# Performance work log

Measured on AMD Instinct MI355X. Metric: run time of the kernel, lower is better.

The kernel has to match this reference:

```python
import jax, jax.numpy as jnp
import numpy as np

B, L, H, SH, C = 32, 512, 1024, 50, 3   # batch, leaves, hidden, hidden_syn_size, num_classes
N = 2 * L - 1                            # total tree nodes (complete binary / heap order)
VOCAB, SYN = 30000, 128
LVLS = int(np.log2(L))                   # number of internal levels (root = level 0)


def _linear(k, fin, fout):
    lim = 1.0 / np.sqrt(fin)
    kw, kb = jax.random.split(k)
    W = jax.random.uniform(kw, (fin, fout), minval=-lim, maxval=lim, dtype=jnp.float32)
    b = jax.random.uniform(kb, (fout,), minval=-lim, maxval=lim, dtype=jnp.float32)
    return W, b


def setup_inputs() -> dict:
    key = jax.random.key(0)
    ks = jax.random.split(key, 12)
    x = jax.random.randint(ks[0], (B, N), 0, SYN)                 # node ids (word at leaves, syntax elsewhere)
    word_index = jnp.broadcast_to(jnp.arange(L - 1, 2 * L - 1), (B, L))  # leaf node indices (heap order)
    cue = jax.random.randint(ks[1], (B, N), 0, C)
    pos = jax.random.randint(ks[2], (B, L), 0, SYN)               # POS tag per leaf
    # parent->child adjacency of the heap tree, adj[:,1] is what forward reads
    A = np.zeros((N, N), dtype=bool)
    par = np.arange(L - 1)
    A[par, 2 * par + 1] = True
    A[par, 2 * par + 2] = True
    adj = jnp.broadcast_to(jnp.asarray(A)[None, None], (B, 2, N, N))
    pre_embs = jnp.zeros((1,), jnp.float32)                       # unused (use_pretrained_embs=False)
    word_emb_W = jax.random.normal(ks[3], (VOCAB, H), jnp.float32) * 0.02
    syn_emb_W = jax.random.normal(ks[4], (SYN, SH), jnp.float32) * 0.02
    leaf_W, leaf_b = _linear(ks[5], H + SH + C, H)
    comp_W, comp_b = _linear(ks[6], 2 * H + SH, H)
    grev_W, grev_b = _linear(ks[7], H + SH, H)
    dec_W, dec_b = _linear(ks[8], 2 * H + 2 * SH, 2 * H)
    clf_W, clf_b = _linear(ks[9], 2 * H, C)
    return dict(x=x, word_index=word_index, cue=cue, adj=adj, pos=pos, pre_embs=pre_embs,
                word_emb_W=word_emb_W, syn_emb_W=syn_emb_W,
                leaf_W=leaf_W, leaf_b=leaf_b, comp_W=comp_W, comp_b=comp_b,
                grev_W=grev_W, grev_b=grev_b, dec_W=dec_W, dec_b=dec_b,
                clf_W=clf_W, clf_b=clf_b)


def reference(x, word_index, cue, adj, pos, pre_embs,
              word_emb_W, syn_emb_W, leaf_W, leaf_b, comp_W, comp_b,
              grev_W, grev_b, dec_W, dec_b, clf_W, clf_b):
    # Eval-mode forward (self.training == False, so no dropout masks are applied).
    # Tree structure is the complete binary heap encoded in adj: children of i are 2i+1, 2i+2.
    b_ix = jnp.arange(B)[:, None]
    s = jnp.take_along_axis(x, word_index, axis=1)                # (B,L) leaf word ids
    c = jnp.take_along_axis(cue, word_index, axis=1)              # (B,L) leaf cue ids
    word_e = word_emb_W[s]                                        # (B,L,H)
    cue_e = jax.nn.one_hot(c, C, dtype=word_e.dtype)              # (B,L,C)
    pos_e = syn_emb_W[pos]                                        # (B,L,SH)
    x_emb = jnp.concatenate([word_e, cue_e, pos_e], -1) @ leaf_W + leaf_b  # (B,L,H), no activation

    up = jnp.zeros((B, N, H), x_emb.dtype).at[b_ix, word_index].set(x_emb)
    # upward pass: batched level-order compose (bottom internal level -> root)
    for lvl in range(LVLS - 1, -1, -1):
        nodes = jnp.arange(2 ** lvl - 1, 2 ** (lvl + 1) - 1)
        l, r = 2 * nodes + 1, 2 * nodes + 2
        cons = syn_emb_W[x[:, nodes]]                             # (B,W,SH)
        ctx = jnp.concatenate([cons, up[:, l], up[:, r]], -1)     # (B,W,SH+2H)
        up = up.at[:, nodes].set(jnp.tanh(ctx @ comp_W + comp_b))

    root_ctx = jnp.concatenate([up[:, 0], syn_emb_W[x[:, 0]]], -1)
    gd = jnp.tanh(root_ctx @ grev_W + grev_b)                     # (B,H)
    down = jnp.zeros((B, N, H), gd.dtype).at[:, 0].set(gd)
    # downward pass: batched level-order decompose (root -> leaves)
    for lvl in range(LVLS):
        nodes = jnp.arange(2 ** lvl - 1, 2 ** (lvl + 1) - 1)
        l, r = 2 * nodes + 1, 2 * nodes + 2
        if lvl == LVLS - 1:   # children are leaves -> their syntax is the POS embedding
            cons_l = pos_e[:, l - (L - 1)]
            cons_r = pos_e[:, r - (L - 1)]
        else:
            cons_l = syn_emb_W[x[:, l]]
            cons_r = syn_emb_W[x[:, r]]
        pctx = jnp.concatenate([down[:, nodes], up[:, nodes]], -1)  # (parent_emb, upward[parent])
        dctx = jnp.concatenate([cons_l, cons_r, pctx], -1)
        ch = jnp.tanh(dctx @ dec_W + dec_b)                        # (B,W,2H)
        down = down.at[:, l].set(ch[..., :H]).at[:, r].set(ch[..., H:])

    tree = jnp.concatenate([down, up], -1)                         # (B,N,2H)
    return jnp.tanh(tree @ clf_W + clf_b)                          # (B,N,C)
```

## Files before the change

kernel.cpp:

```cpp
#include <hip/hip_runtime.h>

typedef unsigned short u16;
typedef unsigned int   u32;

typedef __bf16 bf16x8 __attribute__((ext_vector_type(8)));
typedef float  f32x4  __attribute__((ext_vector_type(4)));

#define NB 1023
#define HH 1024

__device__ __forceinline__ float b2f(u16 x) { return __uint_as_float(((u32)x) << 16); }
__device__ __forceinline__ u16 f2b(float f) {
    u32 u = __float_as_uint(f);
    u += 0x7fffu + ((u >> 16) & 1u);
    return (u16)(u >> 16);
}
__device__ __forceinline__ float fast_tanh(float x) {
    float cx = fminf(fmaxf(x, -12.f), 12.f);
    float e = __expf(2.f * cx);
    return __fdividef(e - 1.f, e + 1.f);
}
__device__ __forceinline__ void async_copy16(const void* gptr, void* lptr) {
    __builtin_amdgcn_global_load_lds((__attribute__((address_space(1))) void*)gptr,
                                     (__attribute__((address_space(3))) void*)lptr,
                                     16, 0, 0);
}
__device__ __forceinline__ u16 loadAsBf16(const void* p, size_t idx, int isf32) {
    if (isf32) return f2b(((const float*)p)[idx]);
    return ((const u16*)p)[idx];
}

__device__ __forceinline__ int detect_local(const u32* __restrict__ w) {
    __shared__ int cnt;
    const int tid = threadIdx.x;
    if (tid == 0) cnt = 0;
    __syncthreads();
    u32 v = w[tid & 255];
    u32 lo = v & 0xFFFFu;
    u32 e = (lo >> 7) & 0xFFu;
    if ((lo != 0u) && (e < 60u || e > 140u)) atomicAdd(&cnt, 1);
    __syncthreads();
    return cnt >= 64;
}

__device__ void conv_range(const void* __restrict__ src, u16* __restrict__ dst,
                           int n, int tbase, int isf32) {
    const int i = ((int)blockIdx.x - tbase) * 256 + threadIdx.x;
    if (i < n) dst[i] = loadAsBf16(src, i, isf32);
}

__device__ void transpose_tile(const void* __restrict__ W, u16* __restrict__ Wt,
                               int Nw, int Kpad, int bx, int by, int isf32,
                               int ps0, int ps1, int ps2, int ps3,
                               int os0, int os1, int os2, int os3,
                               int ln0, int ln1, int ln2, int ln3)
{
    __shared__ u16 tile[32][33];
    const int tid = threadIdx.x;
    const int tx = tid & 31, ty = tid >> 5;
    #pragma unroll
    for (int i = 0; i < 4; ++i) {
        const int kp = by*32 + ty + i*8;
        const int n = bx*32 + tx;
        int ko = -1;
        if      (kp >= ps0 && kp < ps0 + ln0) ko = os0 + (kp - ps0);
        else if (kp >= ps1 && kp < ps1 + ln1) ko = os1 + (kp - ps1);
        else if (kp >= ps2 && kp < ps2 + ln2) ko = os2 + (kp - ps2);
        else if (kp >= ps3 && kp < ps3 + ln3) ko = os3 + (kp - ps3);
        u16 v = 0;
        if (ko >= 0) v = loadAsBf16(W, (size_t)ko * Nw + n, isf32);
        tile[ty + i*8][tx] = v;
    }
    __syncthreads();
    #pragma unroll
    for (int i = 0; i < 4; ++i) {
        const int n = bx*32 + ty + i*8;
        const int kp = by*32 + tx;
        Wt[(size_t)n * Kpad + kp] = tile[tx][ty + i*8];
    }
}

__global__ __launch_bounds__(256)
void preprocess(const u32* __restrict__ wembU,
                const int* __restrict__ x, const int* __restrict__ cue,
                const int* __restrict__ pos,
                const void* __restrict__ semb,  const void* __restrict__ leafb,
                const void* __restrict__ compb, const void* __restrict__ grevb,
                const void* __restrict__ decb,  const void* __restrict__ clfb,
                const void* __restrict__ clfW,
                const void* __restrict__ leafW, const void* __restrict__ compW,
                const void* __restrict__ grevW, const void* __restrict__ decW,
                u16* __restrict__ sembP,  u16* __restrict__ leafbC,
                u16* __restrict__ compbC, u16* __restrict__ grevbC,
                u16* __restrict__ decbC,  u16* __restrict__ clfbC,
                u16* __restrict__ clfWC,
                u16* __restrict__ leafWt, u16* __restrict__ compWt,
                u16* __restrict__ grevWt, u16* __restrict__ decWt,
                u16* __restrict__ ctx)
{
    const int isf32 = detect_local(wembU);
    const int bid = blockIdx.x;
    if (bid < 32) {
        const int i = bid * 256 + threadIdx.x;
        const int s = i >> 6, c = i & 63;
        sembP[i] = (c < 50) ? loadAsBf16(semb, s * 50 + c, isf32) : (u16)0;
    } else if (bid < 36)  conv_range(leafb, leafbC, 1024, 32, isf32);
    else if (bid < 40)  conv_range(compb, compbC, 1024, 36, isf32);
    else if (bid < 44)  conv_range(grevb, grevbC, 1024, 40, isf32);
    else if (bid < 52)  conv_range(decb,  decbC,  2048, 44, isf32);
    else if (bid < 53)  conv_range(clfb,  clfbC,  3,    52, isf32);
    else if (bid < 77)  conv_range(clfW,  clfWC,  6144, 53, isf32);
    else if (bid < 1165) {
        const int t = bid - 77;
        transpose_tile(leafW, leafWt, 1024, 1088, t & 31, t >> 5, isf32,
                       0,-1,-1,-1,  0,0,0,0,  1077,0,0,0);
    } else if (bid < 3277) {
        const int t = bid - 1165;
        transpose_tile(compW, compWt, 1024, 2112, t & 31, t >> 5, isf32,
                       0,64,1088,-1,  0,50,1074,0,  50,1024,1024,0);
    } else if (bid < 4365) {
        const int t = bid - 3277;
        transpose_tile(grevW, grevWt, 1024, 1088, t & 31, t >> 5, isf32,
                       0,1024,-1,-1,  0,1024,0,0,  1024,50,0,0);
    } else if (bid < 8717) {
        const int t = bid - 4365;
        transpose_tile(decW, decWt, 2048, 2176, t & 63, t >> 6, isf32,
                       0,64,128,1152,  0,50,100,1124,  50,50,1024,1024);
    } else {
        const int m = bid - 8717;
        const int b = m >> 9, i = m & 511;
        const int node = 511 + i;
        const int s  = x[b*NB + node];
        const int cv = cue[b*NB + node];
        const int p  = pos[b*512 + i];
        u16* row = ctx + (size_t)m * 1088;
        u32* row32 = (u32*)row;
        const int tid = threadIdx.x;
        if (isf32) {
            const float2* wrf = ((const float2*)wembU) + (size_t)s * 512;
            for (int c = tid; c < 512; c += 256) {
                float2 t = wrf[c];
                row32[c] = (u32)f2b(t.x) | ((u32)f2b(t.y) << 16);
            }
        } else {
            const u32* wr = ((const u32*)wembU) + (size_t)s * 512;
            for (int c = tid; c < 512; c += 256) row32[c] = wr[c];
        }
        if (tid < 64) {
            const int c = tid;
            u16 v;
            if (c < 3)       v = (c == cv) ? (u16)0x3F80 : (u16)0;
            else if (c < 53) v = loadAsBf16(semb, p * 50 + (c - 3), isf32);
            else             v = 0;
            row[1024 + c] = v;
        }
    }
}

template<int AKIND>
__device__ __forceinline__ void setup_arows(
    int mrow, int M, int nodeBase, int lognn, int mask, int leafLvl, int scol, int Kpad,
    const u16* __restrict__ actx, const int* __restrict__ x, const int* __restrict__ pos,
    const u16* __restrict__ sembP, const u16* __restrict__ upB, const u16* __restrict__ downB,
    const u16*& q0, const u16*& q1, const u16*& q2, const u16*& q3)
{
    const int mr = (mrow < M) ? mrow : 0;
    if (AKIND == 0) {
        q0 = actx + (size_t)mr * Kpad + scol;
    } else if (AKIND == 1) {
        const int b_ = mr >> lognn, ii = mr & mask;
        const int node = nodeBase + ii;
        const int s = x[b_*NB + node];
        q0 = sembP + s*64 + scol;
        q1 = upB + (((size_t)(b_*NB + 2*node + 1)) << 10) + scol;
        q2 = upB + (((size_t)(b_*NB + 2*node + 2)) << 10) + scol;
    } else if (AKIND == 2) {
        q0 = upB + (((size_t)(mr*NB)) << 10) + scol;
        q1 = sembP + x[mr*NB]*64 + scol;
    } else {
        const int b_ = mr >> lognn, ii = mr & mask;
        const int node = nodeBase + ii;
        const int l = 2*node + 1, r = l + 1;
        int sli, sri;
        if (leafLvl) { sli = pos[b_*512 + (l-511)]; sri = pos[b_*512 + (r-511)]; }
        else         { sli = x[b_*NB + l]; sri = x[b_*NB + r]; }
        q0 = sembP + sli*64 + scol;
        q1 = sembP + sri*64 + scol;
        q2 = downB + (((size_t)(b_*NB + node)) << 10) + scol;
        q3 = upB   + (((size_t)(b_*NB + node)) << 10) + scol;
    }
}

template<int AKIND, int MODE>
__global__ __launch_bounds__(256)
void gemm_fused(const u16* __restrict__ Bt, const u16* __restrict__ bias,
                u16* __restrict__ dst, int M, int Kpad, int nodeBase, int lognn,
                int leafLvl,
                const u16* __restrict__ actx,
                const int* __restrict__ x, const int* __restrict__ pos,
                const u16* __restrict__ sembP,
                const u16* __restrict__ upB, const u16* __restrict__ downB)
{
    __shared__ __align__(16) u16 As[2*4096];
    __shared__ __align__(16) u16 Bs[2*4096];
    const int tid  = threadIdx.x;
    const int wave = tid >> 6;
    const int lane = tid & 63;
    const int bm = blockIdx.y << 7;
    const int bn = blockIdx.x << 7;
    const int wm = (wave & 1) << 6;
    const int wn = (wave >> 1) << 6;
    const int quad = lane >> 4;
    const int l16  = lane & 15;
    const int srow = lane >> 2;
    const int scol = (lane & 3) << 3;
    const int mask = (1 << lognn) - 1;

    const u16 *p0[2], *p1[2], *p2[2], *p3[2];
    #pragma unroll
    for (int h = 0; h < 2; ++h)
        setup_arows<AKIND>(bm + wave*16 + srow + h*64, M, nodeBase, lognn, mask, leafLvl,
                           scol, Kpad, actx, x, pos, sembP, upB, downB,
                           p0[h], p1[h], p2[h], p3[h]);

    const u16* gB0 = Bt + (size_t)(bn + wave*16 + srow) * Kpad + scol;
    const u16* gB1 = gB0 + (size_t)64 * Kpad;
    u16* lA0 = &As[wave * 512];
    u16* lA1 = &As[(wave + 4) * 512];
    u16* lB0 = &Bs[wave * 512];
    u16* lB1 = &Bs[(wave + 4) * 512];

    const u16* pa[4]; const u16* pb[4];
    #pragma unroll
    for (int i = 0; i < 4; ++i) pa[i] = &As[(wm + i*16 + l16) * 32 + quad*8];
    #pragma unroll
    for (int j = 0; j < 4; ++j) pb[j] = &Bs[(wn + j*16 + l16) * 32 + quad*8];

    f32x4 zero4 = {0.f, 0.f, 0.f, 0.f};
    f32x4 acc[4][4];
    #pragma unroll
    for (int i = 0; i < 4; ++i)
        #pragma unroll
        for (int j = 0; j < 4; ++j) acc[i][j] = zero4;

    auto kstep64 = [&](const u16* sA0, const u16* sA1, int k0) {
        async_copy16(sA0,           lA0);
        async_copy16(sA1,           lA1);
        async_copy16(gB0 + k0,      lB0);
        async_copy16(gB1 + k0,      lB1);
        async_copy16(sA0 + 32,      lA0 + 4096);
        async_copy16(sA1 + 32,      lA1 + 4096);
        async_copy16(gB0 + k0 + 32, lB0 + 4096);
        async_copy16(gB1 + k0 + 32, lB1 + 4096);
        __syncthreads();
        #pragma unroll
        for (int c = 0; c < 2; ++c) {
            bf16x8 a[4], b[4];
            #pragma unroll
            for (int i = 0; i < 4; ++i) a[i] = *(const bf16x8*)(pa[i] + c*4096);
            #pragma unroll
            for (int j = 0; j < 4; ++j) b[j] = *(const bf16x8*)(pb[j] + c*4096);
            #pragma unroll
            for (int i = 0; i < 4; ++i)
                #pragma unroll
                for (int j = 0; j < 4; ++j)
                    acc[i][j] = __builtin_amdgcn_mfma_f32_16x16x32_bf16(a[i], b[j], acc[i][j], 0, 0, 0);
        }
        __syncthreads();
    };

    if (AKIND == 0) {
        for (int k0 = 0; k0 < 1088; k0 += 64) kstep64(p0[0] + k0, p0[1] + k0, k0);
    } else if (AKIND == 1) {
        kstep64(p0[0], p0[1], 0);
        for (int k0 = 64;   k0 < 1088; k0 += 64) kstep64(p1[0] + (k0-64),   p1[1] + (k0-64),   k0);
        for (int k0 = 1088; k0 < 2112; k0 += 64) kstep64(p2[0] + (k0-1088), p2[1] + (k0-1088), k0);
    } else if (AKIND == 2) {
        for (int k0 = 0; k0 < 1024; k0 += 64) kstep64(p0[0] + k0, p0[1] + k0, k0);
        kstep64(p1[0], p1[1], 1024);
    } else {
        kstep64(p0[0], p0[1], 0);
        kstep64(p1[0], p1[1], 64);
        for (int k0 = 128;  k0 < 1152; k0 += 64) kstep64(p2[0] + (k0-128),  p2[1] + (k0-128),  k0);
        for (int k0 = 1152; k0 < 2176; k0 += 64) kstep64(p3[0] + (k0-1152), p3[1] + (k0-1152), k0);
    }

    #pragma unroll
    for (int i = 0; i < 4; ++i) {
        #pragma unroll
        for (int j = 0; j < 4; ++j) {
            const int gn = bn + wn + j*16 + l16;
            const float bv = b2f(bias[gn]);
            #pragma unroll
            for (int r = 0; r < 4; ++r) {
                const int gm = bm + wm + i*16 + quad*4 + r;
                if (gm < M) {
                    float v = acc[i][j][r] + bv;
                    if (MODE != 0) v = fast_tanh(v);
                    const int b_ = gm >> lognn;
                    const int ii = gm & mask;
                    const int node = nodeBase + ii;
                    size_t addr;
                    if (MODE == 2) {
                        const int child = 2*node + 1 + (gn >> 10);
                        addr = (((size_t)(b_*NB + child)) << 10) + (gn & 1023);
                    } else {
                        addr = (((size_t)(b_*NB + node)) << 10) + gn;
                    }
                    dst[addr] = f2b(v);
                }
            }
        }
    }
}

template<int AKIND, int MODE>
__global__ __launch_bounds__(256, 2)
void gemm_wide(const u16* __restrict__ Bt, const u16* __restrict__ bias,
               u16* __restrict__ dst, int M, int Kpad, int nodeBase, int lognn,
               int leafLvl,
               const u16* __restrict__ actx,
               const int* __restrict__ x, const int* __restrict__ pos,
               const u16* __restrict__ sembP,
               const u16* __restrict__ upB, const u16* __restrict__ downB)
{
    __shared__ __align__(16) u16 As[2*4096];
    __shared__ __align__(16) u16 Bs[2*8192];
    const int tid  = threadIdx.x;
    const int wave = tid >> 6;
    const int lane = tid & 63;
    const int bm = blockIdx.y << 7;
    const int bn = blockIdx.x << 8;
    const int wm = (wave & 1) << 6;
    const int wn = (wave >> 1) << 7;
    const int quad = lane >> 4;
    const int l16  = lane & 15;
    const int srow = lane >> 2;
    const int scol = (lane & 3) << 3;
    const int mask = (1 << lognn) - 1;

    const u16 *p0[2], *p1[2], *p2[2], *p3[2];
    #pragma unroll
    for (int h = 0; h < 2; ++h)
        setup_arows<AKIND>(bm + wave*16 + srow + h*64, M, nodeBase, lognn, mask, leafLvl,
                           scol, Kpad, actx, x, pos, sembP, upB, downB,
                           p0[h], p1[h], p2[h], p3[h]);

    const u16* gB[4];
    #pragma unroll
    for (int g = 0; g < 4; ++g)
        gB[g] = Bt + (size_t)(bn + wave*64 + g*16 + srow) * Kpad + scol;
    u16* lA0 = &As[wave * 512];
    u16* lA1 = &As[(wave + 4) * 512];
    u16* lB[4];
    #pragma unroll
    for (int g = 0; g < 4; ++g) lB[g] = &Bs[wave * 2048 + g * 512];

    const u16* pa[4]; const u16* pb[8];
    #pragma unroll
    for (int i = 0; i < 4; ++i) pa[i] = &As[(wm + i*16 + l16) * 32 + quad*8];
    #pragma unroll
    for (int j = 0; j < 8; ++j) pb[j] = &Bs[(wn + j*16 + l16) * 32 + quad*8];

    f32x4 zero4 = {0.f, 0.f, 0.f, 0.f};
    f32x4 acc[4][8];
    #pragma unroll
    for (int i = 0; i < 4; ++i)
        #pragma unroll
        for (int j = 0; j < 8; ++j) acc[i][j] = zero4;

    auto kstep64 = [&](const u16* sA0, const u16* sA1, int k0) {
        async_copy16(sA0,      lA0);
        async_copy16(sA1,      lA1);
        #pragma unroll
        for (int g = 0; g < 4; ++g) async_copy16(gB[g] + k0, lB[g]);
        async_copy16(sA0 + 32, lA0 + 4096);
        async_copy16(sA1 + 32, lA1 + 4096);
        #pragma unroll
        for (int g = 0; g < 4; ++g) async_copy16(gB[g] + k0 + 32, lB[g] + 8192);
        __syncthreads();
        #pragma unroll
        for (int c = 0; c < 2; ++c) {
            bf16x8 a[4], b[8];
            #pragma unroll
            for (int i = 0; i < 4; ++i) a[i] = *(const bf16x8*)(pa[i] + c*4096);
            #pragma unroll
            for (int j = 0; j < 8; ++j) b[j] = *(const bf16x8*)(pb[j] + c*8192);
            #pragma unroll
            for (int i = 0; i < 4; ++i)
                #pragma unroll
                for (int j = 0; j < 8; ++j)
                    acc[i][j] = __builtin_amdgcn_mfma_f32_16x16x32_bf16(a[i], b[j], acc[i][j], 0, 0, 0);
        }
        __syncthreads();
    };

    if (AKIND == 0) {
        for (int k0 = 0; k0 < 1088; k0 += 64) kstep64(p0[0] + k0, p0[1] + k0, k0);
    } else if (AKIND == 1) {
        kstep64(p0[0], p0[1], 0);
        for (int k0 = 64;   k0 < 1088; k0 += 64) kstep64(p1[0] + (k0-64),   p1[1] + (k0-64),   k0);
        for (int k0 = 1088; k0 < 2112; k0 += 64) kstep64(p2[0] + (k0-1088), p2[1] + (k0-1088), k0);
    } else if (AKIND == 2) {
        for (int k0 = 0; k0 < 1024; k0 += 64) kstep64(p0[0] + k0, p0[1] + k0, k0);
        kstep64(p1[0], p1[1], 1024);
    } else {
        kstep64(p0[0], p0[1], 0);
        kstep64(p1[0], p1[1], 64);
        for (int k0 = 128;  k0 < 1152; k0 += 64) kstep64(p2[0] + (k0-128),  p2[1] + (k0-128),  k0);
        for (int k0 = 1152; k0 < 2176; k0 += 64) kstep64(p3[0] + (k0-1152), p3[1] + (k0-1152), k0);
    }

    #pragma unroll
    for (int i = 0; i < 4; ++i) {
        #pragma unroll
        for (int j = 0; j < 8; ++j) {
            const int gn = bn + wn + j*16 + l16;
            const float bv = b2f(bias[gn]);
            #pragma unroll
            for (int r = 0; r < 4; ++r) {
                const int gm = bm + wm + i*16 + quad*4 + r;
                if (gm < M) {
                    float v = acc[i][j][r] + bv;
                    if (MODE != 0) v = fast_tanh(v);
                    const int b_ = gm >> lognn;
                    const int ii = gm & mask;
                    const int node = nodeBase + ii;
                    size_t addr;
                    if (MODE == 2) {
                        const int child = 2*node + 1 + (gn >> 10);
                        addr = (((size_t)(b_*NB + child)) << 10) + (gn & 1023);
                    } else {
                        addr = (((size_t)(b_*NB + node)) << 10) + gn;
                    }
                    dst[addr] = f2b(v);
                }
            }
        }
    }
}

__global__ __launch_bounds__(256)
void classifier_kernel(const u16* __restrict__ down, const u16* __restrict__ up,
                       const u16* __restrict__ clfW, const u16* __restrict__ clfb,
                       void* __restrict__ outp, const u32* __restrict__ wembU)
{
    __shared__ float wls[3][2048];
    const int isf32 = detect_local(wembU);
    const int tid = threadIdx.x;
    for (int idx = tid; idx < 6144; idx += 256) {
        const int c = idx >> 11, k = idx & 2047;
        wls[c][k] = b2f(clfW[k*3 + c]);
    }
    __syncthreads();
    const int wave = tid >> 6, lane = tid & 63;
    const float b0 = b2f(clfb[0]), b1 = b2f(clfb[1]), b2v = b2f(clfb[2]);
    const int base = blockIdx.x * 32;
    for (int rr = 0; rr < 8; ++rr) {
        const int row = base + rr*4 + wave;
        const u32* dn = (const u32*)(down + ((size_t)row << 10));
        const u32* un = (const u32*)(up   + ((size_t)row << 10));
        float a0 = 0.f, a1 = 0.f, a2 = 0.f;
        #pragma unroll
        for (int t = 0; t < 8; ++t) {
            const int j = t*64 + lane;
            const u32 dp = dn[j], uu = un[j];
            const int k = j*2;
            const float d0 = __uint_as_float(dp << 16);
            const float d1 = __uint_as_float(dp & 0xffff0000u);
            const float u0 = __uint_as_float(uu << 16);
            const float u1 = __uint_as_float(uu & 0xffff0000u);
            a0 += d0*wls[0][k] + d1*wls[0][k+1] + u0*wls[0][1024+k] + u1*wls[0][1025+k];
            a1 += d0*wls[1][k] + d1*wls[1][k+1] + u0*wls[1][1024+k] + u1*wls[1][1025+k];
            a2 += d0*wls[2][k] + d1*wls[2][k+1] + u0*wls[2][1024+k] + u1*wls[2][1025+k];
        }
        #pragma unroll
        for (int off = 32; off; off >>= 1) {
            a0 += __shfl_down(a0, off);
            a1 += __shfl_down(a1, off);
            a2 += __shfl_down(a2, off);
        }
        if (lane == 0) {
            const float v0 = fast_tanh(a0 + b0);
            const float v1 = fast_tanh(a1 + b1);
            const float v2 = fast_tanh(a2 + b2v);
            if (isf32) {
                float* o = (float*)outp + (size_t)row * 3;
                o[0] = v0; o[1] = v1; o[2] = v2;
            } else {
                u16* o = (u16*)outp + (size_t)row * 3;
                o[0] = f2b(v0); o[1] = f2b(v1); o[2] = f2b(v2);
            }
        }
    }
}

extern "C" void kernel_launch(void* const* d_in, const int* in_sizes, int n_in,
                              void* d_out, int out_size, void* d_ws, size_t ws_size,
                              hipStream_t stream)
{
    (void)in_sizes; (void)n_in; (void)out_size; (void)ws_size;
    const int* x    = (const int*)d_in[0];
    const int* cue  = (const int*)d_in[2];
    const int* pos  = (const int*)d_in[4];
    const void* wemb  = d_in[6];
    const void* semb  = d_in[7];
    const void* leafW = d_in[8];
    const void* leafb = d_in[9];
    const void* compW = d_in[10];
    const void* compb = d_in[11];
    const void* grevW = d_in[12];
    const void* grevb = d_in[13];
    const void* decW  = d_in[14];
    const void* decb  = d_in[15];
    const void* clfW  = d_in[16];
    const void* clfb  = d_in[17];

    char* ws = (char*)d_ws;
    u16* up_buf   = (u16*)(ws + 0);
    u16* down_buf = (u16*)(ws + 67043328);
    u16* ctx      = (u16*)(ws + 134086656);
    u16* leafWt   = (u16*)(ws + 169738240);
    u16* compWt   = (u16*)(ws + 171966464);
    u16* grevWt   = (u16*)(ws + 176291840);
    u16* decWt    = (u16*)(ws + 178520064);
    u16* sembP    = (u16*)(ws + 187432960);
    u16* leafbC   = (u16*)(ws + 187449344);
    u16* compbC   = (u16*)(ws + 187451392);
    u16* grevbC   = (u16*)(ws + 187453440);
    u16* decbC    = (u16*)(ws + 187455488);
    u16* clfbC    = (u16*)(ws + 187459584);
    u16* clfWC    = (u16*)(ws + 187459600);

    preprocess<<<25101, 256, 0, stream>>>((const u32*)wemb, x, cue, pos,
        semb, leafb, compb, grevb, decb, clfb, clfW,
        leafW, compW, grevW, decW,
        sembP, leafbC, compbC, grevbC, decbC, clfbC, clfWC,
        leafWt, compWt, grevWt, decWt, ctx);

    gemm_wide<0,0><<<dim3(4, 128), 256, 0, stream>>>(leafWt, leafbC, up_buf,
        16384, 1088, 511, 9, 0, ctx, x, pos, sembP, up_buf, down_buf);
    gemm_wide<1,1><<<dim3(4, 64), 256, 0, stream>>>(compWt, compbC, up_buf,
        8192, 2112, 255, 8, 0, nullptr, x, pos, sembP, up_buf, down_buf);
    for (int lvl = 7; lvl >= 0; --lvl) {
        const int M = 32 << lvl;
        const int Mpad = M < 128 ? 128 : M;
        const int first = (1 << lvl) - 1;
        gemm_fused<1,1><<<dim3(8, Mpad >> 7), 256, 0, stream>>>(compWt, compbC, up_buf,
            M, 2112, first, lvl, 0, nullptr, x, pos, sembP, up_buf, down_buf);
    }
    gemm_fused<2,1><<<dim3(8, 1), 256, 0, stream>>>(grevWt, grevbC, down_buf,
        32, 1088, 0, 0, 0, nullptr, x, pos, sembP, up_buf, down_buf);
    for (int lvl = 0; lvl <= 6; ++lvl) {
        const int M = 32 << lvl;
        const int Mpad = M < 128 ? 128 : M;
        const int first = (1 << lvl) - 1;
        gemm_fused<3,2><<<dim3(16, Mpad >> 7), 256, 0, stream>>>(decWt, decbC, down_buf,
            M, 2176, first, lvl, 0, nullptr, x, pos, sembP, up_buf, down_buf);
    }
    gemm_wide<3,2><<<dim3(8, 32), 256, 0, stream>>>(decWt, decbC, down_buf,
        4096, 2176, 127, 7, 0, nullptr, x, pos, sembP, up_buf, down_buf);
    gemm_wide<3,2><<<dim3(8, 64), 256, 0, stream>>>(decWt, decbC, down_buf,
        8192, 2176, 255, 8, 1, nullptr, x, pos, sembP, up_buf, down_buf);
    classifier_kernel<<<1023, 256, 0, stream>>>(down_buf, up_buf, clfWC, clfbC,
                                                d_out, (const u32*)wemb);
}
```

Before: 1.343 ms.

## Merge small tree-level GEMMs into persistent kernel with grid barriers

Replaces the sixteen small per-level GEMM launches (upward compose levels 7..0, root decompose, downward levels 0..6) with one persistent 256-block kernel. The kernel walks the phases itself and separates them with an atomic global barrier, removing launch gaps and tail idle time between dependent levels. The large leaf, compose and last decompose GEMMs also move from the 128x256 wide tile to the 128x128 fused kernel. The tile routine now takes its mode as a runtime argument, which may cost registers and branch overhead. The barrier relies on all 256 blocks being co-resident.

```diff
diff --git a/kernel.cpp b/kernel.cpp
--- a/kernel.cpp
+++ b/kernel.cpp
@@ -41,6 +41,24 @@
     if ((lo != 0u) && (e < 60u || e > 140u)) atomicAdd(&cnt, 1);
     __syncthreads();
     return cnt >= 64;
+}
+
+__device__ __forceinline__ void gbar(u32* cnt, u32* gen, u32 nb) {
+    __threadfence();
+    __syncthreads();
+    if (threadIdx.x == 0) {
+        u32 g = __hip_atomic_load(gen, __ATOMIC_RELAXED, __HIP_MEMORY_SCOPE_AGENT);
+        u32 old = __hip_atomic_fetch_add(cnt, 1u, __ATOMIC_ACQ_REL, __HIP_MEMORY_SCOPE_AGENT);
+        if (old == nb - 1u) {
+            __hip_atomic_store(cnt, 0u, __ATOMIC_RELAXED, __HIP_MEMORY_SCOPE_AGENT);
+            __hip_atomic_store(gen, g + 1u, __ATOMIC_RELEASE, __HIP_MEMORY_SCOPE_AGENT);
+        } else {
+            while (__hip_atomic_load(gen, __ATOMIC_ACQUIRE, __HIP_MEMORY_SCOPE_AGENT) == g)
+                __builtin_amdgcn_s_sleep(2);
+        }
+    }
+    __syncthreads();
+    __threadfence();
 }
 
 __device__ void conv_range(const void* __restrict__ src, u16* __restrict__ dst,
@@ -96,10 +114,11 @@
                 u16* __restrict__ clfWC,
                 u16* __restrict__ leafWt, u16* __restrict__ compWt,
                 u16* __restrict__ grevWt, u16* __restrict__ decWt,
-                u16* __restrict__ ctx)
+                u16* __restrict__ ctx, u32* __restrict__ barWS)
 {
     const int isf32 = detect_local(wembU);
     const int bid = blockIdx.x;
+    if (bid == 0 && threadIdx.x < 32) barWS[threadIdx.x] = 0;
     if (bid < 32) {
         const int i = bid * 256 + threadIdx.x;
         const int s = i >> 6, c = i & 63;
@@ -314,25 +333,18 @@
     }
 }
 
-template<int AKIND, int MODE>
-__global__ __launch_bounds__(256, 2)
-void gemm_wide(const u16* __restrict__ Bt, const u16* __restrict__ bias,
-               u16* __restrict__ dst, int M, int Kpad, int nodeBase, int lognn,
-               int leafLvl,
-               const u16* __restrict__ actx,
-               const int* __restrict__ x, const int* __restrict__ pos,
-               const u16* __restrict__ sembP,
-               const u16* __restrict__ upB, const u16* __restrict__ downB)
-{
-    __shared__ __align__(16) u16 As[2*4096];
-    __shared__ __align__(16) u16 Bs[2*8192];
+__device__ void tile_gemm_rt(int akind, int mode, int bm, int bn,
+    int M, int Kpad, int nodeBase, int lognn,
+    const u16* __restrict__ Bt, const u16* __restrict__ bias, u16* __restrict__ dst,
+    const int* __restrict__ x, const u16* __restrict__ sembP,
+    const u16* __restrict__ upB, const u16* __restrict__ downB,
+    u16* As, u16* Bs)
+{
     const int tid  = threadIdx.x;
     const int wave = tid >> 6;
     const int lane = tid & 63;
-    const int bm = blockIdx.y << 7;
-    const int bn = blockIdx.x << 8;
     const int wm = (wave & 1) << 6;
-    const int wn = (wave >> 1) << 7;
+    const int wn = (wave >> 1) << 6;
     const int quad = lane >> 4;
     const int l16  = lane & 15;
     const int srow = lane >> 2;
@@ -341,93 +353,102 @@
 
     const u16 *p0[2], *p1[2], *p2[2], *p3[2];
     #pragma unroll
-    for (int h = 0; h < 2; ++h)
-        setup_arows<AKIND>(bm + wave*16 + srow + h*64, M, nodeBase, lognn, mask, leafLvl,
-                           scol, Kpad, actx, x, pos, sembP, upB, downB,
-                           p0[h], p1[h], p2[h], p3[h]);
-
-    const u16* gB[4];
-    #pragma unroll
-    for (int g = 0; g < 4; ++g)
-        gB[g] = Bt + (size_t)(bn + wave*64 + g*16 + srow) * Kpad + scol;
+    for (int h = 0; h < 2; ++h) {
+        const int mrow = bm + wave*16 + srow + h*64;
+        const int mr = (mrow < M) ? mrow : 0;
+        if (akind == 1) {
+            const int b_ = mr >> lognn, ii = mr & mask;
+            const int node = nodeBase + ii;
+            p0[h] = sembP + x[b_*NB + node]*64 + scol;
+            p1[h] = upB + (((size_t)(b_*NB + 2*node + 1)) << 10) + scol;
+            p2[h] = upB + (((size_t)(b_*NB + 2*node + 2)) << 10) + scol;
+            p3[h] = p0[h];
+        } else if (akind == 2) {
+            p0[h] = upB + (((size_t)(mr*NB)) << 10) + scol;
+            p1[h] = sembP + x[mr*NB]*64 + scol;
+            p2[h] = p0[h]; p3[h] = p0[h];
+        } else {
+            const int b_ = mr >> lognn, ii = mr & mask;
+            const int node = nodeBase + ii;
+            p0[h] = sembP + x[b_*NB + 2*node + 1]*64 + scol;
+            p1[h] = sembP + x[b_*NB + 2*node + 2]*64 + scol;
+            p2[h] = downB + (((size_t)(b_*NB + node)) << 10) + scol;
+            p3[h] = upB   + (((size_t)(b_*NB + node)) << 10) + scol;
+        }
+    }
+
+    const u16* gB0 = Bt + (size_t)(bn + wave*16 + srow) * Kpad + scol;
+    const u16* gB1 = gB0 + (size_t)64 * Kpad;
     u16* lA0 = &As[wave * 512];
     u16* lA1 = &As[(wave + 4) * 512];
-    u16* lB[4];
-    #pragma unroll
-    for (int g = 0; g < 4; ++g) lB[g] = &Bs[wave * 2048 + g * 512];
-
-    const u16* pa[4]; const u16* pb[8];
+    u16* lB0 = &Bs[wave * 512];
+    u16* lB1 = &Bs[(wave + 4) * 512];
+
+    const u16* pa[4]; const u16* pb[4];
     #pragma unroll
     for (int i = 0; i < 4; ++i) pa[i] = &As[(wm + i*16 + l16) * 32 + quad*8];
     #pragma unroll
-    for (int j = 0; j < 8; ++j) pb[j] = &Bs[(wn + j*16 + l16) * 32 + quad*8];
+    for (int j = 0; j < 4; ++j) pb[j] = &Bs[(wn + j*16 + l16) * 32 + quad*8];
 
     f32x4 zero4 = {0.f, 0.f, 0.f, 0.f};
-    f32x4 acc[4][8];
+    f32x4 acc[4][4];
     #pragma unroll
     for (int i = 0; i < 4; ++i)
         #pragma unroll
-        for (int j = 0; j < 8; ++j) acc[i][j] = zero4;
-
-    auto kstep64 = [&](const u16* sA0, const u16* sA1, int k0) {
-        async_copy16(sA0,      lA0);
-        async_copy16(sA1,      lA1);
-        #pragma unroll
-        for (int g = 0; g < 4; ++g) async_copy16(gB[g] + k0, lB[g]);
-        async_copy16(sA0 + 32, lA0 + 4096);
-        async_copy16(sA1 + 32, lA1 + 4096);
-        #pragma unroll
-        for (int g = 0; g < 4; ++g) async_copy16(gB[g] + k0 + 32, lB[g] + 8192);
+        for (int j = 0; j < 4; ++j) acc[i][j] = zero4;
+
+    int k0 = 0;
+    auto kstep64 = [&](const u16* sA0, const u16* sA1) {
+        async_copy16(sA0,           lA0);
+        async_copy16(sA1,           lA1);
+        async_copy16(gB0 + k0,      lB0);
+        async_copy16(gB1 + k0,      lB1);
+        async_copy16(sA0 + 32,      lA0 + 4096);
+        async_copy16(sA1 + 32,      lA1 + 4096);
+        async_copy16(gB0 + k0 + 32, lB0 + 4096);
+        async_copy16(gB1 + k0 + 32, lB1 + 4096);
         __syncthreads();
         #pragma unroll
         for (int c = 0; c < 2; ++c) {
-            bf16x8 a[4], b[8];
+            bf16x8 a[4], b[4];
             #pragma unroll
             for (int i = 0; i < 4; ++i) a[i] = *(const bf16x8*)(pa[i] + c*4096);
             #pragma unroll
-            for (int j = 0; j < 8; ++j) b[j] = *(const bf16x8*)(pb[j] + c*8192);
+            for (int j = 0; j < 4; ++j) b[j] = *(const bf16x8*)(pb[j] + c*4096);
             #pragma unroll
             for (int i = 0; i < 4; ++i)
                 #pragma unroll
-                for (int j = 0; j < 8; ++j)
+                for (int j = 0; j < 4; ++j)
                     acc[i][j] = __builtin_amdgcn_mfma_f32_16x16x32_bf16(a[i], b[j], acc[i][j], 0, 0, 0);
         }
         __syncthreads();
+        k0 += 64;
     };
-
-    if (AKIND == 0) {
-        for (int k0 = 0; k0 < 1088; k0 += 64) kstep64(p0[0] + k0, p0[1] + k0, k0);
-    } else if (AKIND == 1) {
-        kstep64(p0[0], p0[1], 0);
-        for (int k0 = 64;   k0 < 1088; k0 += 64) kstep64(p1[0] + (k0-64),   p1[1] + (k0-64),   k0);
-        for (int k0 = 1088; k0 < 2112; k0 += 64) kstep64(p2[0] + (k0-1088), p2[1] + (k0-1088), k0);
-    } else if (AKIND == 2) {
-        for (int k0 = 0; k0 < 1024; k0 += 64) kstep64(p0[0] + k0, p0[1] + k0, k0);
-        kstep64(p1[0], p1[1], 1024);
-    } else {
-        kstep64(p0[0], p0[1], 0);
-        kstep64(p1[0], p1[1], 64);
-        for (int k0 = 128;  k0 < 1152; k0 += 64) kstep64(p2[0] + (k0-128),  p2[1] + (k0-128),  k0);
-        for (int k0 = 1152; k0 < 2176; k0 += 64) kstep64(p3[0] + (k0-1152), p3[1] + (k0-1152), k0);
-    }
+    auto seg = [&](const u16* a0, const u16* a1, int L) {
+        for (int kk = 0; kk < L; kk += 64) kstep64(a0 + kk, a1 + kk);
+    };
+
+    if (akind == 1)      { seg(p0[0],p0[1],64); seg(p1[0],p1[1],1024); seg(p2[0],p2[1],1024); }
+    else if (akind == 2) { seg(p0[0],p0[1],1024); seg(p1[0],p1[1],64); }
+    else                 { seg(p0[0],p0[1],64); seg(p1[0],p1[1],64);
+                           seg(p2[0],p2[1],1024); seg(p3[0],p3[1],1024); }
 
     #pragma unroll
     for (int i = 0; i < 4; ++i) {
         #pragma unroll
-        for (int j = 0; j < 8; ++j) {
+        for (int j = 0; j < 4; ++j) {
             const int gn = bn + wn + j*16 + l16;
             const float bv = b2f(bias[gn]);
             #pragma unroll
             for (int r = 0; r < 4; ++r) {
                 const int gm = bm + wm + i*16 + quad*4 + r;
                 if (gm < M) {
-                    float v = acc[i][j][r] + bv;
-                    if (MODE != 0) v = fast_tanh(v);
+                    float v = fast_tanh(acc[i][j][r] + bv);
                     const int b_ = gm >> lognn;
                     const int ii = gm & mask;
                     const int node = nodeBase + ii;
                     size_t addr;
-                    if (MODE == 2) {
+                    if (mode == 2) {
                         const int child = 2*node + 1 + (gn >> 10);
                         addr = (((size_t)(b_*NB + child)) << 10) + (gn & 1023);
                     } else {
@@ -437,6 +458,45 @@
                 }
             }
         }
+    }
+}
+
+__global__ __launch_bounds__(256)
+void tree_mega(const u16* __restrict__ compWt, const u16* __restrict__ compbC,
+               const u16* __restrict__ grevWt, const u16* __restrict__ grevbC,
+               const u16* __restrict__ decWt,  const u16* __restrict__ decbC,
+               u16* __restrict__ upB, u16* __restrict__ downB,
+               const int* __restrict__ x, const u16* __restrict__ sembP,
+               u32* __restrict__ barCnt, u32* __restrict__ barGen)
+{
+    __shared__ __align__(16) u16 As[2*4096];
+    __shared__ __align__(16) u16 Bs[2*4096];
+    const u32 nb = gridDim.x;
+    for (int ph = 0; ph < 16; ++ph) {
+        int akind, mode, M, Kpad, nodeBase, lognn, Ntiles;
+        const u16 *Bt, *bias; u16* dst;
+        if (ph < 8) {
+            const int lvl = 7 - ph;
+            akind = 1; mode = 1; M = 32 << lvl; Kpad = 2112;
+            nodeBase = (1 << lvl) - 1; lognn = lvl; Ntiles = 8;
+            Bt = compWt; bias = compbC; dst = upB;
+        } else if (ph == 8) {
+            akind = 2; mode = 1; M = 32; Kpad = 1088;
+            nodeBase = 0; lognn = 0; Ntiles = 8;
+            Bt = grevWt; bias = grevbC; dst = downB;
+        } else {
+            const int lvl = ph - 9;
+            akind = 3; mode = 2; M = 32 << lvl; Kpad = 2176;
+            nodeBase = (1 << lvl) - 1; lognn = lvl; Ntiles = 16;
+            Bt = decWt; bias = decbC; dst = downB;
+        }
+        const int Mtiles = (M + 127) >> 7;
+        const int t = (int)blockIdx.x;
+        if (t < Mtiles * Ntiles)
+            tile_gemm_rt(akind, mode, (t / Ntiles) << 7, (t % Ntiles) << 7,
+                         M, Kpad, nodeBase, lognn, Bt, bias, dst,
+                         x, sembP, upB, downB, As, Bs);
+        gbar(barCnt, barGen, nb);
     }
 }
 
@@ -531,36 +591,24 @@
     u16* decbC    = (u16*)(ws + 187455488);
     u16* clfbC    = (u16*)(ws + 187459584);
     u16* clfWC    = (u16*)(ws + 187459600);
+    u32* barWS    = (u32*)(ws + 187472000);
 
     preprocess<<<25101, 256, 0, stream>>>((const u32*)wemb, x, cue, pos,
         semb, leafb, compb, grevb, decb, clfb, clfW,
         leafW, compW, grevW, decW,
         sembP, leafbC, compbC, grevbC, decbC, clfbC, clfWC,
-        leafWt, compWt, grevWt, decWt, ctx);
-
-    gemm_wide<0,0><<<dim3(4, 128), 256, 0, stream>>>(leafWt, leafbC, up_buf,
+        leafWt, compWt, grevWt, decWt, ctx, barWS);
+
+    gemm_fused<0,0><<<dim3(8, 128), 256, 0, stream>>>(leafWt, leafbC, up_buf,
         16384, 1088, 511, 9, 0, ctx, x, pos, sembP, up_buf, down_buf);
-    gemm_wide<1,1><<<dim3(4, 64), 256, 0, stream>>>(compWt, compbC, up_buf,
+    gemm_fused<1,1><<<dim3(8, 64), 256, 0, stream>>>(compWt, compbC, up_buf,
         8192, 2112, 255, 8, 0, nullptr, x, pos, sembP, up_buf, down_buf);
-    for (int lvl = 7; lvl >= 0; --lvl) {
-        const int M = 32 << lvl;
-        const int Mpad = M < 128 ? 128 : M;
-        const int first = (1 << lvl) - 1;
-        gemm_fused<1,1><<<dim3(8, Mpad >> 7), 256, 0, stream>>>(compWt, compbC, up_buf,
-            M, 2112, first, lvl, 0, nullptr, x, pos, sembP, up_buf, down_buf);
-    }
-    gemm_fused<2,1><<<dim3(8, 1), 256, 0, stream>>>(grevWt, grevbC, down_buf,
-        32, 1088, 0, 0, 0, nullptr, x, pos, sembP, up_buf, down_buf);
-    for (int lvl = 0; lvl <= 6; ++lvl) {
-        const int M = 32 << lvl;
-        const int Mpad = M < 128 ? 128 : M;
-        const int first = (1 << lvl) - 1;
-        gemm_fused<3,2><<<dim3(16, Mpad >> 7), 256, 0, stream>>>(decWt, decbC, down_buf,
-            M, 2176, first, lvl, 0, nullptr, x, pos, sembP, up_buf, down_buf);
-    }
-    gemm_wide<3,2><<<dim3(8, 32), 256, 0, stream>>>(decWt, decbC, down_buf,
+    tree_mega<<<256, 256, 0, stream>>>(compWt, compbC, grevWt, grevbC, decWt, decbC,
+                                       up_buf, down_buf, x, sembP,
+                                       &barWS[0], &barWS[16]);
+    gemm_fused<3,2><<<dim3(16, 32), 256, 0, stream>>>(decWt, decbC, down_buf,
         4096, 2176, 127, 7, 0, nullptr, x, pos, sembP, up_buf, down_buf);
-    gemm_wide<3,2><<<dim3(8, 64), 256, 0, stream>>>(decWt, decbC, down_buf,
+    gemm_fused<3,2><<<dim3(16, 64), 256, 0, stream>>>(decWt, decbC, down_buf,
         8192, 2176, 255, 8, 1, nullptr, x, pos, sembP, up_buf, down_buf);
     classifier_kernel<<<1023, 256, 0, stream>>>(down_buf, up_buf, clfWC, clfbC,
                                                 d_out, (const u32*)wemb);
```

After: 3.681 ms. 174% more time.

## Swizzle LDS tiles, add direct-load GEMM for small levels, drop wide kernel

Applied to the files above, without the earlier changes.

Applies an XOR swizzle to the LDS staging layout in gemm_fused to avoid bank conflicts on fragment reads. Replaces gemm_wide with gemm_direct, which loads MFMA operands straight from global memory without LDS or barriers; it is used for the small tree levels (M up to 2048) and the root decompose. The large leaf, composition and decomposition levels now use gemm_fused with a 128x128 tile instead of 128x256, which doubles the grid. The aim is lower latency on small, launch-bound levels and fewer LDS conflicts. The cost is less operand reuse and more global traffic per MFMA in the direct kernel.

```diff
diff --git a/kernel.cpp b/kernel.cpp
--- a/kernel.cpp
+++ b/kernel.cpp
@@ -213,17 +213,19 @@
     const int quad = lane >> 4;
     const int l16  = lane & 15;
     const int srow = lane >> 2;
-    const int scol = (lane & 3) << 3;
+    const int scol4 = lane & 3;
+    const int swz  = ((scol4 ^ ((srow >> 1) & 3)) << 3);
+    const int perm = ((quad ^ ((l16 >> 1) & 3)) << 3);
     const int mask = (1 << lognn) - 1;
 
     const u16 *p0[2], *p1[2], *p2[2], *p3[2];
     #pragma unroll
     for (int h = 0; h < 2; ++h)
         setup_arows<AKIND>(bm + wave*16 + srow + h*64, M, nodeBase, lognn, mask, leafLvl,
-                           scol, Kpad, actx, x, pos, sembP, upB, downB,
+                           swz, Kpad, actx, x, pos, sembP, upB, downB,
                            p0[h], p1[h], p2[h], p3[h]);
 
-    const u16* gB0 = Bt + (size_t)(bn + wave*16 + srow) * Kpad + scol;
+    const u16* gB0 = Bt + (size_t)(bn + wave*16 + srow) * Kpad + swz;
     const u16* gB1 = gB0 + (size_t)64 * Kpad;
     u16* lA0 = &As[wave * 512];
     u16* lA1 = &As[(wave + 4) * 512];
@@ -232,9 +234,9 @@
 
     const u16* pa[4]; const u16* pb[4];
     #pragma unroll
-    for (int i = 0; i < 4; ++i) pa[i] = &As[(wm + i*16 + l16) * 32 + quad*8];
-    #pragma unroll
-    for (int j = 0; j < 4; ++j) pb[j] = &Bs[(wn + j*16 + l16) * 32 + quad*8];
+    for (int i = 0; i < 4; ++i) pa[i] = &As[(wm + i*16 + l16) * 32 + perm];
+    #pragma unroll
+    for (int j = 0; j < 4; ++j) pb[j] = &Bs[(wn + j*16 + l16) * 32 + perm];
 
     f32x4 zero4 = {0.f, 0.f, 0.f, 0.f};
     f32x4 acc[4][4];
@@ -315,106 +317,74 @@
 }
 
 template<int AKIND, int MODE>
-__global__ __launch_bounds__(256, 2)
-void gemm_wide(const u16* __restrict__ Bt, const u16* __restrict__ bias,
-               u16* __restrict__ dst, int M, int Kpad, int nodeBase, int lognn,
-               int leafLvl,
-               const u16* __restrict__ actx,
-               const int* __restrict__ x, const int* __restrict__ pos,
-               const u16* __restrict__ sembP,
-               const u16* __restrict__ upB, const u16* __restrict__ downB)
-{
-    __shared__ __align__(16) u16 As[2*4096];
-    __shared__ __align__(16) u16 Bs[2*8192];
+__global__ __launch_bounds__(256)
+void gemm_direct(const u16* __restrict__ Bt, const u16* __restrict__ bias,
+                 u16* __restrict__ dst, int M, int Kpad, int nodeBase, int lognn,
+                 int leafLvl,
+                 const int* __restrict__ x, const int* __restrict__ pos,
+                 const u16* __restrict__ sembP,
+                 const u16* __restrict__ upB, const u16* __restrict__ downB)
+{
     const int tid  = threadIdx.x;
     const int wave = tid >> 6;
     const int lane = tid & 63;
     const int bm = blockIdx.y << 7;
-    const int bn = blockIdx.x << 8;
+    const int bn = blockIdx.x << 7;
     const int wm = (wave & 1) << 6;
-    const int wn = (wave >> 1) << 7;
+    const int wn = (wave >> 1) << 6;
     const int quad = lane >> 4;
     const int l16  = lane & 15;
-    const int srow = lane >> 2;
-    const int scol = (lane & 3) << 3;
+    const int koff = quad << 3;
     const int mask = (1 << lognn) - 1;
 
-    const u16 *p0[2], *p1[2], *p2[2], *p3[2];
-    #pragma unroll
-    for (int h = 0; h < 2; ++h)
-        setup_arows<AKIND>(bm + wave*16 + srow + h*64, M, nodeBase, lognn, mask, leafLvl,
-                           scol, Kpad, actx, x, pos, sembP, upB, downB,
-                           p0[h], p1[h], p2[h], p3[h]);
-
-    const u16* gB[4];
-    #pragma unroll
-    for (int g = 0; g < 4; ++g)
-        gB[g] = Bt + (size_t)(bn + wave*64 + g*16 + srow) * Kpad + scol;
-    u16* lA0 = &As[wave * 512];
-    u16* lA1 = &As[(wave + 4) * 512];
-    u16* lB[4];
-    #pragma unroll
-    for (int g = 0; g < 4; ++g) lB[g] = &Bs[wave * 2048 + g * 512];
-
-    const u16* pa[4]; const u16* pb[8];
-    #pragma unroll
-    for (int i = 0; i < 4; ++i) pa[i] = &As[(wm + i*16 + l16) * 32 + quad*8];
-    #pragma unroll
-    for (int j = 0; j < 8; ++j) pb[j] = &Bs[(wn + j*16 + l16) * 32 + quad*8];
+    const u16 *q0[4], *q1[4], *q2[4], *q3[4];
+    #pragma unroll
+    for (int i = 0; i < 4; ++i)
+        setup_arows<AKIND>(bm + wm + i*16 + l16, M, nodeBase, lognn, mask, leafLvl,
+                           koff, Kpad, nullptr, x, pos, sembP, upB, downB,
+                           q0[i], q1[i], q2[i], q3[i]);
+
+    const u16* pB[4];
+    #pragma unroll
+    for (int j = 0; j < 4; ++j)
+        pB[j] = Bt + (size_t)(bn + wn + j*16 + l16) * Kpad + koff;
 
     f32x4 zero4 = {0.f, 0.f, 0.f, 0.f};
-    f32x4 acc[4][8];
+    f32x4 acc[4][4];
     #pragma unroll
     for (int i = 0; i < 4; ++i)
         #pragma unroll
-        for (int j = 0; j < 8; ++j) acc[i][j] = zero4;
-
-    auto kstep64 = [&](const u16* sA0, const u16* sA1, int k0) {
-        async_copy16(sA0,      lA0);
-        async_copy16(sA1,      lA1);
-        #pragma unroll
-        for (int g = 0; g < 4; ++g) async_copy16(gB[g] + k0, lB[g]);
-        async_copy16(sA0 + 32, lA0 + 4096);
-        async_copy16(sA1 + 32, lA1 + 4096);
-        #pragma unroll
-        for (int g = 0; g < 4; ++g) async_copy16(gB[g] + k0 + 32, lB[g] + 8192);
-        __syncthreads();
-        #pragma unroll
-        for (int c = 0; c < 2; ++c) {
-            bf16x8 a[4], b[8];
-            #pragma unroll
-            for (int i = 0; i < 4; ++i) a[i] = *(const bf16x8*)(pa[i] + c*4096);
-            #pragma unroll
-            for (int j = 0; j < 8; ++j) b[j] = *(const bf16x8*)(pb[j] + c*8192);
+        for (int j = 0; j < 4; ++j) acc[i][j] = zero4;
+
+    auto kloop = [&](const u16* const* qa, int kbase, int len) {
+        #pragma unroll 2
+        for (int k0 = 0; k0 < len; k0 += 32) {
+            bf16x8 a[4], b[4];
+            #pragma unroll
+            for (int i = 0; i < 4; ++i) a[i] = *(const bf16x8*)(qa[i] + k0);
+            #pragma unroll
+            for (int j = 0; j < 4; ++j) b[j] = *(const bf16x8*)(pB[j] + kbase + k0);
             #pragma unroll
             for (int i = 0; i < 4; ++i)
                 #pragma unroll
-                for (int j = 0; j < 8; ++j)
+                for (int j = 0; j < 4; ++j)
                     acc[i][j] = __builtin_amdgcn_mfma_f32_16x16x32_bf16(a[i], b[j], acc[i][j], 0, 0, 0);
         }
-        __syncthreads();
     };
 
-    if (AKIND == 0) {
-        for (int k0 = 0; k0 < 1088; k0 += 64) kstep64(p0[0] + k0, p0[1] + k0, k0);
-    } else if (AKIND == 1) {
-        kstep64(p0[0], p0[1], 0);
-        for (int k0 = 64;   k0 < 1088; k0 += 64) kstep64(p1[0] + (k0-64),   p1[1] + (k0-64),   k0);
-        for (int k0 = 1088; k0 < 2112; k0 += 64) kstep64(p2[0] + (k0-1088), p2[1] + (k0-1088), k0);
+    if (AKIND == 1) {
+        kloop(q0, 0, 64); kloop(q1, 64, 1024); kloop(q2, 1088, 1024);
     } else if (AKIND == 2) {
-        for (int k0 = 0; k0 < 1024; k0 += 64) kstep64(p0[0] + k0, p0[1] + k0, k0);
-        kstep64(p1[0], p1[1], 1024);
+        kloop(q0, 0, 1024); kloop(q1, 1024, 64);
     } else {
-        kstep64(p0[0], p0[1], 0);
-        kstep64(p1[0], p1[1], 64);
-        for (int k0 = 128;  k0 < 1152; k0 += 64) kstep64(p2[0] + (k0-128),  p2[1] + (k0-128),  k0);
-        for (int k0 = 1152; k0 < 2176; k0 += 64) kstep64(p3[0] + (k0-1152), p3[1] + (k0-1152), k0);
+        kloop(q0, 0, 64); kloop(q1, 64, 64);
+        kloop(q2, 128, 1024); kloop(q3, 1152, 1024);
     }
 
     #pragma unroll
     for (int i = 0; i < 4; ++i) {
         #pragma unroll
-        for (int j = 0; j < 8; ++j) {
+        for (int j = 0; j < 4; ++j) {
             const int gn = bn + wn + j*16 + l16;
             const float bv = b2f(bias[gn]);
             #pragma unroll
@@ -538,29 +508,31 @@
         sembP, leafbC, compbC, grevbC, decbC, clfbC, clfWC,
         leafWt, compWt, grevWt, decWt, ctx);
 
-    gemm_wide<0,0><<<dim3(4, 128), 256, 0, stream>>>(leafWt, leafbC, up_buf,
+    gemm_fused<0,0><<<dim3(8, 128), 256, 0, stream>>>(leafWt, leafbC, up_buf,
         16384, 1088, 511, 9, 0, ctx, x, pos, sembP, up_buf, down_buf);
-    gemm_wide<1,1><<<dim3(4, 64), 256, 0, stream>>>(compWt, compbC, up_buf,
+    gemm_fused<1,1><<<dim3(8, 64), 256, 0, stream>>>(compWt, compbC, up_buf,
         8192, 2112, 255, 8, 0, nullptr, x, pos, sembP, up_buf, down_buf);
-    for (int lvl = 7; lvl >= 0; --lvl) {
+    gemm_fused<1,1><<<dim3(8, 32), 256, 0, stream>>>(compWt, compbC, up_buf,
+        4096, 2112, 127, 7, 0, nullptr, x, pos, sembP, up_buf, down_buf);
+    for (int lvl = 6; lvl >= 0; --lvl) {
         const int M = 32 << lvl;
         const int Mpad = M < 128 ? 128 : M;
         const int first = (1 << lvl) - 1;
-        gemm_fused<1,1><<<dim3(8, Mpad >> 7), 256, 0, stream>>>(compWt, compbC, up_buf,
-            M, 2112, first, lvl, 0, nullptr, x, pos, sembP, up_buf, down_buf);
-    }
-    gemm_fused<2,1><<<dim3(8, 1), 256, 0, stream>>>(grevWt, grevbC, down_buf,
-        32, 1088, 0, 0, 0, nullptr, x, pos, sembP, up_buf, down_buf);
+        gemm_direct<1,1><<<dim3(8, Mpad >> 7), 256, 0, stream>>>(compWt, compbC, up_buf,
+            M, 2112, first, lvl, 0, x, pos, sembP, up_buf, down_buf);
+    }
+    gemm_direct<2,1><<<dim3(8, 1), 256, 0, stream>>>(grevWt, grevbC, down_buf,
+        32, 1088, 0, 0, 0, x, pos, sembP, up_buf, down_buf);
     for (int lvl = 0; lvl <= 6; ++lvl) {
         const int M = 32 << lvl;
         const int Mpad = M < 128 ? 128 : M;
         const int first = (1 << lvl) - 1;
-        gemm_fused<3,2><<<dim3(16, Mpad >> 7), 256, 0, stream>>>(decWt, decbC, down_buf,
-            M, 2176, first, lvl, 0, nullptr, x, pos, sembP, up_buf, down_buf);
-    }
-    gemm_wide<3,2><<<dim3(8, 32), 256, 0, stream>>>(decWt, decbC, down_buf,
+        gemm_direct<3,2><<<dim3(16, Mpad >> 7), 256, 0, stream>>>(decWt, decbC, down_buf,
+            M, 2176, first, lvl, 0, x, pos, sembP, up_buf, down_buf);
+    }
+    gemm_fused<3,2><<<dim3(16, 32), 256, 0, stream>>>(decWt, decbC, down_buf,
         4096, 2176, 127, 7, 0, nullptr, x, pos, sembP, up_buf, down_buf);
-    gemm_wide<3,2><<<dim3(8, 64), 256, 0, stream>>>(decWt, decbC, down_buf,
+    gemm_fused<3,2><<<dim3(16, 64), 256, 0, stream>>>(decWt, decbC, down_buf,
         8192, 2176, 255, 8, 1, nullptr, x, pos, sembP, up_buf, down_buf);
     classifier_kernel<<<1023, 256, 0, stream>>>(down_buf, up_buf, clfWC, clfbC,
                                                 d_out, (const u32*)wemb);
```

After: 1.827 ms. 1.36x slower.
